# Performance work log

Measured on AMD Instinct MI355X. Metric: run time of the kernel, lower is better.

Reference implementation:

```python
import jax, jax.numpy as jnp
import numpy as np

L, H, D, HS = 6, 8, 512, 64
EPS = 1e-5


def _ln(x, g, b):
    m = jnp.mean(x, -1, keepdims=True)
    v = jnp.mean((x - m) ** 2, -1, keepdims=True)
    return (x - m) * jax.lax.rsqrt(v + EPS) * g + b


def _posenc(T, C):
    pos = jnp.arange(T, dtype=jnp.float32)[:, None]
    div = jnp.exp(jnp.arange(0, C, 2, dtype=jnp.float32) * (-jnp.log(10000.0) / C))
    pe = jnp.zeros((T, C), jnp.float32)
    pe = pe.at[:, 0::2].set(jnp.sin(pos * div))
    pe = pe.at[:, 1::2].set(jnp.cos(pos * div))
    return pe


def setup_inputs() -> dict:
    B, T, F, V, E, O = 8, 1024, 32, 7, 16, 49
    key = jax.random.key(0)
    ks = jax.random.split(key, 16)
    s = 0.02
    inp = {
        'code': jax.random.randint(ks[0], (B, T, F), 0, V),
        'lengths': jax.random.randint(ks[1], (B,), T // 2, T + 1),
        'emb': s * jax.random.normal(ks[2], (V, E), jnp.float32),
        'Wq': s * jax.random.normal(ks[3], (L, H, D, HS), jnp.float32),
        'Wk': s * jax.random.normal(ks[4], (L, H, D, HS), jnp.float32),
        'Wv': s * jax.random.normal(ks[5], (L, H, D, HS), jnp.float32),
        'Wo': s * jax.random.normal(ks[6], (L, D, D), jnp.float32),
        'bo': jnp.zeros((L, D), jnp.float32),
        'W1': s * jax.random.normal(ks[7], (L, D, 4 * D), jnp.float32),
        'b1': jnp.zeros((L, 4 * D), jnp.float32),
        'W2': s * jax.random.normal(ks[8], (L, 4 * D, D), jnp.float32),
        'b2': jnp.zeros((L, D), jnp.float32),
        'ln1_g': jnp.ones((L, D), jnp.float32),
        'ln1_b': jnp.zeros((L, D), jnp.float32),
        'ln2_g': jnp.ones((L, D), jnp.float32),
        'ln2_b': jnp.zeros((L, D), jnp.float32),
        'lnf_g': jnp.ones((D,), jnp.float32),
        'lnf_b': jnp.zeros((D,), jnp.float32),
        'attn_w': s * jax.random.normal(ks[9], (D, 1), jnp.float32),
        'attn_b': jnp.zeros((1,), jnp.float32),
        'head_w': s * jax.random.normal(ks[10], (D, 49), jnp.float32),
        'head_b': jnp.zeros((49,), jnp.float32),
    }
    return inp


def reference(code, lengths, emb, Wq, Wk, Wv, Wo, bo, W1, b1, W2, b2,
              ln1_g, ln1_b, ln2_g, ln2_b, lnf_g, lnf_b,
              attn_w, attn_b, head_w, head_b):
    B, T, F = code.shape
    # token embedding (B,T,F,E) -> (B,T,D) plus sinusoidal positions
    x = emb[code].reshape(B, T, D) + _posenc(T, D)
    mask = jnp.arange(T) < lengths[:, None]          # (B,T) valid positions
    col_mask = mask[:, None, None, :]                # mask key columns
    row_mask = mask[:, None, :, None]                # zero padded query rows
    for l in range(L):
        xn = _ln(x, ln1_g[l], ln1_b[l])
        q = jnp.einsum('btd,hde->bhte', xn, Wq[l])
        k = jnp.einsum('btd,hde->bhte', xn, Wk[l])
        v = jnp.einsum('btd,hde->bhte', xn, Wv[l])
        wei = jnp.einsum('bhte,bhse->bhts', q, k) * (HS ** -0.5)
        wei = jnp.where(col_mask, wei, -jnp.inf)
        wei = jax.nn.softmax(wei, axis=-1)
        wei = jnp.where(row_mask, wei, 0.0)
        o = jnp.einsum('bhts,bhse->bthe', wei, v).reshape(B, T, H * HS)
        x = x + o @ Wo[l] + bo[l]
        xn = _ln(x, ln2_g[l], ln2_b[l])
        x = x + jax.nn.gelu(xn @ W1[l] + b1[l], approximate=False) @ W2[l] + b2[l]
    x = _ln(x, lnf_g, lnf_b)
    # attention pooling over time
    scores = x @ attn_w + attn_b                     # (B,T,1)
    scores = jnp.where(mask[:, :, None], scores, -jnp.inf)
    aw = jax.nn.softmax(scores, axis=1)
    summary = jnp.sum(aw * x, axis=1)                # (B,D)
    logits = summary @ head_w + head_b               # (B,49)
    return logits
```

## Files before the change

kernel.cpp:

```cpp
#include <hip/hip_runtime.h>
#include <math.h>

#define TT 1024
#define BB 8
#define DD 512
#define HH 8
#define HSZ 64
#define LL 6
#define FF4 2048

typedef __attribute__((ext_vector_type(8))) short short8;
typedef __attribute__((ext_vector_type(4))) float floatx4;
typedef unsigned short ushort_t;
typedef unsigned int uint_t;

__device__ __forceinline__ ushort_t f2bf(float f) {
  uint_t u = __float_as_uint(f);
  u += 0x7fff + ((u >> 16) & 1);
  return (ushort_t)(u >> 16);
}
__device__ __forceinline__ float bf2f(ushort_t h) {
  return __uint_as_float(((uint_t)h) << 16);
}

typedef const __attribute__((address_space(1))) uint_t* gas_t;
typedef __attribute__((address_space(3))) uint_t* las_t;
__device__ __forceinline__ void stage16(const ushort_t* g, ushort_t* l) {
  __builtin_amdgcn_global_load_lds((gas_t)g, (las_t)l, 16, 0, 0);
}

#define VMWAIT(n) asm volatile("s_waitcnt vmcnt(" #n ")" ::: "memory")
#define MEMFENCE() asm volatile("" ::: "memory")


__global__ __launch_bounds__(256) void k_embed(const int* __restrict__ code,
                                               const float* __restrict__ emb,
                                               float* __restrict__ x,
                                               const int* __restrict__ lengths) {
  int idx = blockIdx.x * 256 + threadIdx.x;
  int c = idx & (DD - 1);
  int bt = idx >> 9;
  int t = bt & (TT - 1);
  if (t >= lengths[bt >> 10]) return;
  int f = c >> 4, e = c & 15;
  int vv = code[bt * 32 + f];
  int i = c >> 1;
  float freq = expf((float)(2 * i) * (-9.210340371976184f / 512.f));
  float ang = (float)t * freq;
  float pe = (c & 1) ? cosf(ang) : sinf(ang);
  x[idx] = emb[vv * 16 + e] + pe;
}

__global__ __launch_bounds__(256) void k_ln(const float* __restrict__ x,
                                            ushort_t* __restrict__ yB,
                                            float* __restrict__ yF,
                                            const float* __restrict__ g,
                                            const float* __restrict__ b,
                                            const float* __restrict__ aw,
                                            const float* __restrict__ ab,
                                            float* __restrict__ scores,
                                            const int* __restrict__ lengths) {
  int row0 = blockIdx.x * 4;
  if ((row0 & (TT - 1)) >= lengths[row0 >> 10]) return;
  int wave = threadIdx.x >> 6, lane = threadIdx.x & 63;
  int row = row0 + wave;
  const float* xr = x + (size_t)row * DD;
  float v[8];
  *(float4*)&v[0] = *(const float4*)(xr + lane * 8);
  *(float4*)&v[4] = *(const float4*)(xr + lane * 8 + 4);
  float s = 0.f;
#pragma unroll
  for (int j = 0; j < 8; ++j) s += v[j];
#pragma unroll
  for (int off = 32; off; off >>= 1) s += __shfl_down(s, off, 64);
  float mean = __shfl(s, 0, 64) * (1.f / DD);
  float qv = 0.f;
#pragma unroll
  for (int j = 0; j < 8; ++j) { float d = v[j] - mean; qv += d * d; }
#pragma unroll
  for (int off = 32; off; off >>= 1) qv += __shfl_down(qv, off, 64);
  float rs = rsqrtf(__shfl(qv, 0, 64) * (1.f / DD) + 1e-5f);
  float ov[8];
  float sdot = 0.f;
#pragma unroll
  for (int e = 0; e < 8; ++e) {
    int c = lane * 8 + e;
    ov[e] = (v[e] - mean) * rs * g[c] + b[c];
    if (scores) sdot += ov[e] * aw[c];
  }
  if (yB) {
    short8 o8;
#pragma unroll
    for (int e = 0; e < 8; ++e) o8[e] = (short)f2bf(ov[e]);
    size_t ad = (((size_t)(row >> 4) * 16 + (lane >> 2)) << 9) + ((lane & 3) * 16 + (row & 15)) * 8;
    *(short8*)(yB + ad) = o8;
  } else {
    float* yr = yF + (size_t)row * DD + lane * 8;
    *(float4*)yr = *(float4*)&ov[0];
    *(float4*)(yr + 4) = *(float4*)&ov[4];
  }
  if (scores) {
#pragma unroll
    for (int off = 32; off; off >>= 1) sdot += __shfl_down(sdot, off, 64);
    if (lane == 0) scores[row] = sdot + ab[0];
  }
}

__global__ __launch_bounds__(256) void k_packw(const float* __restrict__ in,
                                               ushort_t* __restrict__ out,
                                               int Nin, long in_ms, int nh,
                                               long os_l, int nblk, int Kout) {
  __shared__ float t4[64][65];
  int mz = blockIdx.z;
  const float* ip = in + (size_t)mz * in_ms;
  ushort_t* op = out + (size_t)(mz / nh) * os_l;
  int nbase = (mz % nh) * nblk + blockIdx.y * 64;
  int k0 = blockIdx.x * 64;
  int cc = threadIdx.x & 63, r0 = threadIdx.x >> 6;
#pragma unroll
  for (int i = 0; i < 16; ++i) {
    int r = r0 * 16 + i;
    t4[r][cc] = ip[(size_t)(k0 + r) * Nin + (nbase - (mz % nh) * nblk) + cc];
  }
  __syncthreads();
#pragma unroll
  for (int half = 0; half < 2; ++half) {
    int c = threadIdx.x + half * 256;
    int joct = c >> 6, nl = c & 63;
    int n = nbase + nl, k = k0 + joct * 8;
    short8 v8;
#pragma unroll
    for (int e = 0; e < 8; ++e) v8[e] = (short)f2bf(t4[joct * 8 + e][nl]);
    size_t ad = (((size_t)(n >> 4) * (Kout >> 5) + (k >> 5)) << 9) + (((k >> 3) & 3) * 16 + (n & 15)) * 8;
    *(short8*)(op + ad) = v8;
  }
}

template <int BM, int BN>
__global__ __launch_bounds__(256, (BM == 128) ? 3 : 4) void k_agemm(const ushort_t* __restrict__ Apk,
                                                                    const ushort_t* __restrict__ Bpk,
                                                                    const float* __restrict__ resid,
                                                                    const float* __restrict__ bias,
                                                                    float* __restrict__ outF,
                                                                    ushort_t* __restrict__ outB,
                                                                    int M, int N, int K, int mode,
                                                                    const int* __restrict__ lengths) {
  constexpr int MT = BM / 32;
  constexpr int NT = BN / 32;
  constexpr int NA = BM / 16;
  constexpr int NB = BN / 16;
  constexpr int NFRAG = NA + NB;
  constexpr int NF = NFRAG / 4;
  constexpr int BUFU = NFRAG * 512;
  constexpr int NBUF = (BM == 128) ? 2 : 4;
  __shared__ ushort_t lds[(BM == 128) ? 20480 : NBUF * BUFU];

  const int tid = threadIdx.x;
  const int w = tid >> 6, lane = tid & 63;
  const int quad = lane >> 4, l16 = lane & 15;
  const int gx = N / BN;
  int id = blockIdx.x;
  int bx = (id >> 3) % gx;
  int by = (id / (8 * gx)) * 8 + (id & 7);
  const int row0 = by * BM, col0 = bx * BN;
  if (lengths && (row0 & (TT - 1)) >= lengths[row0 >> 10]) return;
  const int nk = K >> 5;

  const int wrow0 = row0 + (w >> 1) * (BM / 2);
  const int wcol0 = col0 + (w & 1) * (BN / 2);
  const int ar16 = (w >> 1) * MT;
  const int bc16 = NA + (w & 1) * NT;

  const ushort_t* gsrc[NF];
  int slot[NF];
#pragma unroll
  for (int i = 0; i < NF; ++i) {
    int f = w * NF + i;
    if (f < NA)
      gsrc[i] = Apk + (((size_t)((row0 >> 4) + f) * nk) << 9) + lane * 8;
    else
      gsrc[i] = Bpk + (((size_t)((col0 >> 4) + (f - NA)) * nk) << 9) + lane * 8;
    slot[i] = f * 512;
  }

  floatx4 acc[MT][NT] = {};

  auto computeStep = [&](int bb) {
    const int base = bb * BUFU;
    short8 af[MT], bfv[NT];
#pragma unroll
    for (int mt = 0; mt < MT; ++mt) af[mt] = *(const short8*)&lds[base + (ar16 + mt) * 512 + lane * 8];
#pragma unroll
    for (int nt = 0; nt < NT; ++nt) bfv[nt] = *(const short8*)&lds[base + (bc16 + nt) * 512 + lane * 8];
#pragma unroll
    for (int mt = 0; mt < MT; ++mt)
#pragma unroll
      for (int nt = 0; nt < NT; ++nt)
        acc[mt][nt] = __builtin_amdgcn_mfma_f32_16x16x32_bf16(af[mt], bfv[nt], acc[mt][nt], 0, 0, 0);
  };

#pragma unroll
  for (int p = 0; p < NBUF - 1; ++p)
#pragma unroll
    for (int i = 0; i < NF; ++i)
      stage16(gsrc[i] + ((size_t)p << 9), &lds[p * BUFU + slot[i]]);

  int kc = 0;
  for (; kc + NBUF - 1 < nk; ++kc) {
    const int sslot = (kc + NBUF - 1) & (NBUF - 1);
#pragma unroll
    for (int i = 0; i < NF; ++i)
      stage16(gsrc[i] + ((size_t)(kc + NBUF - 1) << 9), &lds[sslot * BUFU + slot[i]]);
    if constexpr (BM == 128) VMWAIT(4);
    else VMWAIT(6);
    __builtin_amdgcn_s_barrier();
    MEMFENCE();
    computeStep(kc & (NBUF - 1));
    MEMFENCE();
    __builtin_amdgcn_s_barrier();
  }
  if constexpr (NBUF == 2) {
    VMWAIT(0);
    __builtin_amdgcn_s_barrier();
    MEMFENCE();
    computeStep(kc & 1);
  } else {
    VMWAIT(4);
    __builtin_amdgcn_s_barrier();
    MEMFENCE();
    computeStep(kc & 3);
    VMWAIT(2);
    __builtin_amdgcn_s_barrier();
    MEMFENCE();
    computeStep((kc + 1) & 3);
    VMWAIT(0);
    __builtin_amdgcn_s_barrier();
    MEMFENCE();
    computeStep((kc + 2) & 3);
  }

  if (BM == 128 && mode == 2) {
    __syncthreads();
    ushort_t* Cb = &lds[w * 5120];
#pragma unroll
    for (int mt = 0; mt < MT; ++mt)
#pragma unroll
      for (int nt = 0; nt < NT; ++nt) {
        floatx4 a4 = acc[mt][nt];
#pragma unroll
        for (int r = 0; r < 4; ++r) {
          float val = a4[r] + bias[wcol0 + nt * 16 + l16];
          val = 0.5f * val * (1.f + erff(val * 0.7071067811865475f));
          Cb[(mt * 16 + quad * 4 + r) * 80 + nt * 16 + l16] = f2bf(val);
        }
      }
#pragma unroll
    for (int mt2 = 0; mt2 < 4; ++mt2)
#pragma unroll
      for (int kt2 = 0; kt2 < 2; ++kt2) {
        short8 v8 = *(const short8*)&Cb[(mt2 * 16 + l16) * 80 + kt2 * 32 + quad * 8];
        size_t ad = ((((size_t)(wrow0 >> 4) + mt2) * (N >> 5) + (wcol0 >> 5) + kt2) << 9) + lane * 8;
        *(short8*)(outB + ad) = v8;
      }
  } else {
    const float qscale = (mode == 3 && col0 < 512) ? 0.125f : 1.0f;
#pragma unroll
    for (int mt = 0; mt < MT; ++mt)
#pragma unroll
      for (int nt = 0; nt < NT; ++nt) {
        floatx4 a4 = acc[mt][nt];
#pragma unroll
        for (int r = 0; r < 4; ++r) {
          int row = wrow0 + mt * 16 + quad * 4 + r;
          int col = wcol0 + nt * 16 + l16;
          float val = a4[r];
          if (bias) val += bias[col];
          size_t idx = (size_t)row * N + col;
          if (mode == 1) outF[idx] = val + resid[idx];
          else outB[idx] = f2bf(val * qscale);
        }
      }
  }
}

__global__ __launch_bounds__(256) void k_attn(const ushort_t* __restrict__ qkv,
                                              const int* __restrict__ lengths,
                                              ushort_t* __restrict__ o) {
  __shared__ ushort_t Ks[64 * 72];
  __shared__ ushort_t Vt[64 * 72];
  __shared__ ushort_t Ps[4][16 * 72];
  const int tid = threadIdx.x;
  const int w = tid >> 6, lane = tid & 63;
  const int quad = lane >> 4, l16 = lane & 15;
  const int tile = blockIdx.x & 15;
  const int bh = blockIdx.x >> 4;
  const int b = bh >> 3, h = bh & 7;
  const int len = lengths[b];
  if (tile * 64 >= len) return;
  const int tqa = tile * 64 + w * 16 + l16;
  const ushort_t* qp = qkv + ((size_t)(b * TT + tqa)) * 1536 + h * HSZ + quad * 8;
  short8 qf0 = *(const short8*)qp;
  short8 qf1 = *(const short8*)(qp + 32);
  floatx4 oacc[4] = {};
  float lsum[4] = {0.f, 0.f, 0.f, 0.f};
  const int skey = tid >> 2, sseg = (tid & 3) << 4;
  const int vkp = (tid & 31) << 1, vds = (tid >> 5) << 3;
  const int nkt = (len + 63) >> 6;
  for (int kt = 0; kt < nkt; ++kt) {
    const int s0 = kt * 64;
    __syncthreads();
    {
      const ushort_t* kp = qkv + ((size_t)(b * TT + s0 + skey)) * 1536 + 512 + h * HSZ + sseg;
      short8 k0 = *(const short8*)kp;
      short8 k1 = *(const short8*)(kp + 8);
      *(short8*)&Ks[skey * 72 + sseg] = k0;
      *(short8*)&Ks[skey * 72 + sseg + 8] = k1;
      const ushort_t* vp0 = qkv + ((size_t)(b * TT + s0 + vkp)) * 1536 + 1024 + h * HSZ + vds;
      short8 v0 = *(const short8*)vp0;
      short8 v1 = *(const short8*)(vp0 + 1536);
#pragma unroll
      for (int i = 0; i < 8; ++i) {
        ushort2 pr;
        pr.x = (ushort_t)v0[i];
        pr.y = (ushort_t)v1[i];
        *(ushort2*)&Vt[(vds + i) * 72 + vkp] = pr;
      }
    }
    __syncthreads();
    floatx4 sacc[4] = {};
#pragma unroll
    for (int nt = 0; nt < 4; ++nt) {
      short8 kf0 = *(const short8*)&Ks[(nt * 16 + l16) * 72 + quad * 8];
      short8 kf1 = *(const short8*)&Ks[(nt * 16 + l16) * 72 + 32 + quad * 8];
      sacc[nt] = __builtin_amdgcn_mfma_f32_16x16x32_bf16(qf0, kf0, sacc[nt], 0, 0, 0);
      sacc[nt] = __builtin_amdgcn_mfma_f32_16x16x32_bf16(qf1, kf1, sacc[nt], 0, 0, 0);
    }
    float p[4][4];
    if (kt == nkt - 1) {
#pragma unroll
      for (int nt = 0; nt < 4; ++nt) {
        bool valid = (s0 + nt * 16 + l16 < len);
#pragma unroll
        for (int r = 0; r < 4; ++r) p[nt][r] = valid ? __expf(sacc[nt][r]) : 0.f;
      }
    } else {
#pragma unroll
      for (int nt = 0; nt < 4; ++nt)
#pragma unroll
        for (int r = 0; r < 4; ++r) p[nt][r] = __expf(sacc[nt][r]);
    }
#pragma unroll
    for (int r = 0; r < 4; ++r)
#pragma unroll
      for (int nt = 0; nt < 4; ++nt) {
        lsum[r] += p[nt][r];
        Ps[w][(quad * 4 + r) * 72 + nt * 16 + l16] = f2bf(p[nt][r]);
      }
    short8 pf0 = *(const short8*)&Ps[w][l16 * 72 + quad * 8];
    short8 pf1 = *(const short8*)&Ps[w][l16 * 72 + 32 + quad * 8];
#pragma unroll
    for (int nt = 0; nt < 4; ++nt) {
      short8 vf0 = *(const short8*)&Vt[(nt * 16 + l16) * 72 + quad * 8];
      short8 vf1 = *(const short8*)&Vt[(nt * 16 + l16) * 72 + 32 + quad * 8];
      oacc[nt] = __builtin_amdgcn_mfma_f32_16x16x32_bf16(pf0, vf0, oacc[nt], 0, 0, 0);
      oacc[nt] = __builtin_amdgcn_mfma_f32_16x16x32_bf16(pf1, vf1, oacc[nt], 0, 0, 0);
    }
  }
#pragma unroll
  for (int off = 1; off < 16; off <<= 1) {
#pragma unroll
    for (int r = 0; r < 4; ++r) lsum[r] += __shfl_xor(lsum[r], off, 64);
  }
#pragma unroll
  for (int r = 0; r < 4; ++r) {
    int t = tile * 64 + w * 16 + quad * 4 + r;
    float inv = (t < len) ? 1.f / lsum[r] : 0.f;
#pragma unroll
    for (int nt = 0; nt < 4; ++nt)
      Ps[w][(quad * 4 + r) * 72 + nt * 16 + l16] = f2bf(oacc[nt][r] * inv);
  }
  const int mtile = b * 64 + tile * 4 + w;
#pragma unroll
  for (int kt2 = 0; kt2 < 2; ++kt2) {
    short8 v8 = *(const short8*)&Ps[w][l16 * 72 + kt2 * 32 + quad * 8];
    size_t ad = (((size_t)mtile * 16 + h * 2 + kt2) << 9) + lane * 8;
    *(short8*)(o + ad) = v8;
  }
}

__global__ __launch_bounds__(256) void k_softw(const float* __restrict__ scores,
                                               const int* __restrict__ lengths,
                                               float* __restrict__ wts) {
  __shared__ float red[8];
  int tid = threadIdx.x, b = blockIdx.x;
  int len = lengths[b];
  const float* sb = scores + b * TT;
  float m = -1e30f;
  for (int t = tid; t < len; t += 256) m = fmaxf(m, sb[t]);
#pragma unroll
  for (int off = 32; off; off >>= 1) m = fmaxf(m, __shfl_down(m, off, 64));
  if ((tid & 63) == 0) red[tid >> 6] = m;
  __syncthreads();
  m = fmaxf(fmaxf(red[0], red[1]), fmaxf(red[2], red[3]));
  float ssum = 0.f;
  for (int t = tid; t < len; t += 256) ssum += __expf(sb[t] - m);
#pragma unroll
  for (int off = 32; off; off >>= 1) ssum += __shfl_down(ssum, off, 64);
  if ((tid & 63) == 0) red[4 + (tid >> 6)] = ssum;
  __syncthreads();
  float inv = 1.f / (red[4] + red[5] + red[6] + red[7]);
  for (int t = tid; t < TT; t += 256)
    wts[b * TT + t] = (t < len) ? __expf(sb[t] - m) * inv : 0.f;
}

__global__ __launch_bounds__(256) void k_wsum(const float* __restrict__ xf,
                                              const float* __restrict__ wts,
                                              float* __restrict__ partial,
                                              const int* __restrict__ lengths) {
  int b = blockIdx.x, c = blockIdx.y, tid = threadIdx.x;
  float* pp = partial + ((size_t)b * 16 + c) * DD;
  if (c * 64 >= lengths[b]) {
    pp[tid] = 0.f;
    pp[tid + 256] = 0.f;
    return;
  }
  const float* xb = xf + ((size_t)b * TT + c * 64) * DD;
  const float* wb = wts + b * TT + c * 64;
  float a0 = 0.f, a1 = 0.f;
  for (int t = 0; t < 64; ++t) {
    float wv = wb[t];
    a0 += wv * xb[(size_t)t * DD + tid];
    a1 += wv * xb[(size_t)t * DD + tid + 256];
  }
  pp[tid] = a0;
  pp[tid + 256] = a1;
}

__global__ __launch_bounds__(64) void k_head(const float* __restrict__ partial,
                                             const float* __restrict__ head_w,
                                             const float* __restrict__ head_b,
                                             float* __restrict__ out) {
  __shared__ float ssum[DD];
  int b = blockIdx.x, tid = threadIdx.x;
  for (int d = tid; d < DD; d += 64) {
    float s = 0.f;
#pragma unroll
    for (int c = 0; c < 16; ++c) s += partial[((size_t)b * 16 + c) * DD + d];
    ssum[d] = s;
  }
  __syncthreads();
  if (tid < 49) {
    float s = head_b[tid];
    for (int d = 0; d < DD; ++d) s += ssum[d] * head_w[d * 49 + tid];
    out[b * 49 + tid] = s;
  }
}

extern "C" void kernel_launch(void* const* d_in, const int* in_sizes, int n_in,
                              void* d_out, int out_size, void* d_ws, size_t ws_size,
                              hipStream_t stream) {
  const int* code = (const int*)d_in[0];
  const int* lengths = (const int*)d_in[1];
  const float* emb = (const float*)d_in[2];
  const float* Wq = (const float*)d_in[3];
  const float* Wk = (const float*)d_in[4];
  const float* Wv = (const float*)d_in[5];
  const float* Wo = (const float*)d_in[6];
  const float* bo = (const float*)d_in[7];
  const float* W1 = (const float*)d_in[8];
  const float* b1 = (const float*)d_in[9];
  const float* W2 = (const float*)d_in[10];
  const float* b2 = (const float*)d_in[11];
  const float* ln1_g = (const float*)d_in[12];
  const float* ln1_b = (const float*)d_in[13];
  const float* ln2_g = (const float*)d_in[14];
  const float* ln2_b = (const float*)d_in[15];
  const float* lnf_g = (const float*)d_in[16];
  const float* lnf_b = (const float*)d_in[17];
  const float* attn_w = (const float*)d_in[18];
  const float* attn_b = (const float*)d_in[19];
  const float* head_w = (const float*)d_in[20];
  const float* head_b = (const float*)d_in[21];
  float* out = (float*)d_out;

  const size_t NTOK = (size_t)BB * TT;
  float* x = (float*)d_ws;
  ushort_t* xn = (ushort_t*)(x + NTOK * DD);
  ushort_t* un = xn + NTOK * DD;
  ushort_t* qkv = un;
  ushort_t* h1 = un;
  float* xf = (float*)un;
  ushort_t* wqpk = un + (size_t)NTOK * FF4;
  ushort_t* wopk = wqpk + (size_t)LL * 1536 * 512;
  ushort_t* w1pk = wopk + (size_t)LL * 512 * 512;
  ushort_t* w2pk = w1pk + (size_t)LL * 512 * FF4;
  float* scores = (float*)(w2pk + (size_t)LL * FF4 * 512);
  float* wts = scores + NTOK;
  float* partial = wts + NTOK;

  k_packw<<<dim3(8, 1, 48), 256, 0, stream>>>(Wq, wqpk,              64, (long)512 * 64, 8, (long)1536 * 512, 64, 512);
  k_packw<<<dim3(8, 1, 48), 256, 0, stream>>>(Wk, wqpk + 512 * 512,  64, (long)512 * 64, 8, (long)1536 * 512, 64, 512);
  k_packw<<<dim3(8, 1, 48), 256, 0, stream>>>(Wv, wqpk + 1024 * 512, 64, (long)512 * 64, 8, (long)1536 * 512, 64, 512);
  k_packw<<<dim3(8, 8, 6), 256, 0, stream>>>(Wo, wopk, 512, (long)512 * 512, 1, (long)512 * 512, 0, 512);
  k_packw<<<dim3(8, 32, 6), 256, 0, stream>>>(W1, w1pk, 2048, (long)512 * 2048, 1, (long)2048 * 512, 0, 512);
  k_packw<<<dim3(32, 8, 6), 256, 0, stream>>>(W2, w2pk, 512, (long)2048 * 512, 1, (long)512 * 2048, 0, 2048);

  k_embed<<<dim3((unsigned)((NTOK * DD) / 256)), dim3(256), 0, stream>>>(code, emb, x, lengths);

  for (int l = 0; l < LL; ++l) {
    k_ln<<<dim3(NTOK / 4), 256, 0, stream>>>(x, xn, nullptr, ln1_g + l * DD, ln1_b + l * DD,
                                             nullptr, nullptr, nullptr, lengths);
    k_agemm<128, 128><<<dim3(768), 256, 0, stream>>>(xn, wqpk + (size_t)l * 1536 * 512, nullptr, nullptr,
                                                     nullptr, qkv, (int)NTOK, 1536, 512, 3, lengths);
    k_attn<<<dim3(BB * HH * (TT / 64)), 256, 0, stream>>>(qkv, lengths, xn);
    k_agemm<64, 64><<<dim3(1024), 256, 0, stream>>>(xn, wopk + (size_t)l * 512 * 512, x, bo + l * DD,
                                                    x, nullptr, (int)NTOK, 512, 512, 1, lengths);
    k_ln<<<dim3(NTOK / 4), 256, 0, stream>>>(x, xn, nullptr, ln2_g + l * DD, ln2_b + l * DD,
                                             nullptr, nullptr, nullptr, lengths);
    k_agemm<128, 128><<<dim3(1024), 256, 0, stream>>>(xn, w1pk + (size_t)l * 512 * FF4, nullptr, b1 + l * FF4,
                                                      nullptr, h1, (int)NTOK, FF4, 512, 2, lengths);
    k_agemm<64, 64><<<dim3(1024), 256, 0, stream>>>(h1, w2pk + (size_t)l * FF4 * 512, x, b2 + l * DD,
                                                    x, nullptr, (int)NTOK, 512, 2048, 1, lengths);
  }
  k_ln<<<dim3(NTOK / 4), 256, 0, stream>>>(x, nullptr, xf, lnf_g, lnf_b,
                                           attn_w, attn_b, scores, lengths);
  k_softw<<<dim3(BB), 256, 0, stream>>>(scores, lengths, wts);
  k_wsum<<<dim3(BB, 16), 256, 0, stream>>>(xf, wts, partial, lengths);
  k_head<<<dim3(BB), 64, 0, stream>>>(partial, head_w, head_b, out);
}
```

Baseline: 1.211 ms.

## Use 128x64 tiles for Wo/W2 GEMMs with uniform triple-buffered pipeline

```diff
diff --git a/kernel.cpp b/kernel.cpp
--- a/kernel.cpp
+++ b/kernel.cpp
@@ -137,7 +137,7 @@
 }
 
 template <int BM, int BN>
-__global__ __launch_bounds__(256, (BM == 128) ? 3 : 4) void k_agemm(const ushort_t* __restrict__ Apk,
+__global__ __launch_bounds__(256, (BN == 128) ? 3 : 4) void k_agemm(const ushort_t* __restrict__ Apk,
                                                                     const ushort_t* __restrict__ Bpk,
                                                                     const float* __restrict__ resid,
                                                                     const float* __restrict__ bias,
@@ -152,8 +152,8 @@
   constexpr int NFRAG = NA + NB;
   constexpr int NF = NFRAG / 4;
   constexpr int BUFU = NFRAG * 512;
-  constexpr int NBUF = (BM == 128) ? 2 : 4;
-  __shared__ ushort_t lds[(BM == 128) ? 20480 : NBUF * BUFU];
+  constexpr int NBUF = 3;
+  __shared__ ushort_t lds[NBUF * BUFU];
 
   const int tid = threadIdx.x;
   const int w = tid >> 6, lane = tid & 63;
@@ -205,41 +205,34 @@
     for (int i = 0; i < NF; ++i)
       stage16(gsrc[i] + ((size_t)p << 9), &lds[p * BUFU + slot[i]]);
 
+  int cs = 0, ss = NBUF - 1;
   int kc = 0;
   for (; kc + NBUF - 1 < nk; ++kc) {
-    const int sslot = (kc + NBUF - 1) & (NBUF - 1);
 #pragma unroll
     for (int i = 0; i < NF; ++i)
-      stage16(gsrc[i] + ((size_t)(kc + NBUF - 1) << 9), &lds[sslot * BUFU + slot[i]]);
-    if constexpr (BM == 128) VMWAIT(4);
+      stage16(gsrc[i] + ((size_t)(kc + NBUF - 1) << 9), &lds[ss * BUFU + slot[i]]);
+    if constexpr (NF == 4) VMWAIT(8);
     else VMWAIT(6);
     __builtin_amdgcn_s_barrier();
     MEMFENCE();
-    computeStep(kc & (NBUF - 1));
+    computeStep(cs);
     MEMFENCE();
     __builtin_amdgcn_s_barrier();
-  }
-  if constexpr (NBUF == 2) {
-    VMWAIT(0);
-    __builtin_amdgcn_s_barrier();
-    MEMFENCE();
-    computeStep(kc & 1);
-  } else {
-    VMWAIT(4);
-    __builtin_amdgcn_s_barrier();
-    MEMFENCE();
-    computeStep(kc & 3);
-    VMWAIT(2);
-    __builtin_amdgcn_s_barrier();
-    MEMFENCE();
-    computeStep((kc + 1) & 3);
-    VMWAIT(0);
-    __builtin_amdgcn_s_barrier();
-    MEMFENCE();
-    computeStep((kc + 2) & 3);
-  }
-
-  if (BM == 128 && mode == 2) {
+    cs = (cs + 1 == NBUF) ? 0 : cs + 1;
+    ss = (ss + 1 == NBUF) ? 0 : ss + 1;
+  }
+  if constexpr (NF == 4) VMWAIT(4);
+  else VMWAIT(3);
+  __builtin_amdgcn_s_barrier();
+  MEMFENCE();
+  computeStep(cs);
+  const int cs2 = (cs + 1 == NBUF) ? 0 : cs + 1;
+  VMWAIT(0);
+  __builtin_amdgcn_s_barrier();
+  MEMFENCE();
+  computeStep(cs2);
+
+  if (BN == 128 && mode == 2) {
     __syncthreads();
     ushort_t* Cb = &lds[w * 5120];
 #pragma unroll
@@ -513,13 +506,13 @@
     k_agemm<128, 128><<<dim3(768), 256, 0, stream>>>(xn, wqpk + (size_t)l * 1536 * 512, nullptr, nullptr,
                                                      nullptr, qkv, (int)NTOK, 1536, 512, 3, lengths);
     k_attn<<<dim3(BB * HH * (TT / 64)), 256, 0, stream>>>(qkv, lengths, xn);
-    k_agemm<64, 64><<<dim3(1024), 256, 0, stream>>>(xn, wopk + (size_t)l * 512 * 512, x, bo + l * DD,
+    k_agemm<128, 64><<<dim3(512), 256, 0, stream>>>(xn, wopk + (size_t)l * 512 * 512, x, bo + l * DD,
                                                     x, nullptr, (int)NTOK, 512, 512, 1, lengths);
     k_ln<<<dim3(NTOK / 4), 256, 0, stream>>>(x, xn, nullptr, ln2_g + l * DD, ln2_b + l * DD,
                                              nullptr, nullptr, nullptr, lengths);
     k_agemm<128, 128><<<dim3(1024), 256, 0, stream>>>(xn, w1pk + (size_t)l * 512 * FF4, nullptr, b1 + l * FF4,
                                                       nullptr, h1, (int)NTOK, FF4, 512, 2, lengths);
-    k_agemm<64, 64><<<dim3(1024), 256, 0, stream>>>(h1, w2pk + (size_t)l * FF4 * 512, x, b2 + l * DD,
+    k_agemm<128, 64><<<dim3(512), 256, 0, stream>>>(h1, w2pk + (size_t)l * FF4 * 512, x, b2 + l * DD,
                                                     x, nullptr, (int)NTOK, 512, 2048, 1, lengths);
   }
   k_ln<<<dim3(NTOK / 4), 256, 0, stream>>>(x, nullptr, xf, lnf_g, lnf_b,
```

Measured after the change: 1.296 ms. +7.0%, slower.

## Double-buffer K/V tiles in attention kernel and remap block order

Applied to the files above, without the earlier changes.

```diff
diff --git a/kernel.cpp b/kernel.cpp
--- a/kernel.cpp
+++ b/kernel.cpp
@@ -286,14 +286,15 @@
 __global__ __launch_bounds__(256) void k_attn(const ushort_t* __restrict__ qkv,
                                               const int* __restrict__ lengths,
                                               ushort_t* __restrict__ o) {
-  __shared__ ushort_t Ks[64 * 72];
-  __shared__ ushort_t Vt[64 * 72];
+  __shared__ ushort_t Ks[2][64 * 72];
+  __shared__ ushort_t Vt[2][64 * 72];
   __shared__ ushort_t Ps[4][16 * 72];
   const int tid = threadIdx.x;
   const int w = tid >> 6, lane = tid & 63;
   const int quad = lane >> 4, l16 = lane & 15;
-  const int tile = blockIdx.x & 15;
-  const int bh = blockIdx.x >> 4;
+  const int id = (blockIdx.x & 7) * 128 + (blockIdx.x >> 3);
+  const int tile = id & 15;
+  const int bh = id >> 4;
   const int b = bh >> 3, h = bh & 7;
   const int len = lengths[b];
   if (tile * 64 >= len) return;
@@ -306,32 +307,41 @@
   const int skey = tid >> 2, sseg = (tid & 3) << 4;
   const int vkp = (tid & 31) << 1, vds = (tid >> 5) << 3;
   const int nkt = (len + 63) >> 6;
+
+  short8 k0r, k1r, v0r, v1r;
+  auto loadKV = [&](int kt) {
+    const int s0 = kt * 64;
+    const ushort_t* kp = qkv + ((size_t)(b * TT + s0 + skey)) * 1536 + 512 + h * HSZ + sseg;
+    k0r = *(const short8*)kp;
+    k1r = *(const short8*)(kp + 8);
+    const ushort_t* vp0 = qkv + ((size_t)(b * TT + s0 + vkp)) * 1536 + 1024 + h * HSZ + vds;
+    v0r = *(const short8*)vp0;
+    v1r = *(const short8*)(vp0 + 1536);
+  };
+  auto writeKV = [&](int buf) {
+    *(short8*)&Ks[buf][skey * 72 + sseg] = k0r;
+    *(short8*)&Ks[buf][skey * 72 + sseg + 8] = k1r;
+#pragma unroll
+    for (int i = 0; i < 8; ++i) {
+      ushort2 pr;
+      pr.x = (ushort_t)v0r[i];
+      pr.y = (ushort_t)v1r[i];
+      *(ushort2*)&Vt[buf][(vds + i) * 72 + vkp] = pr;
+    }
+  };
+
+  loadKV(0);
+  writeKV(0);
+  __syncthreads();
+  int cur = 0;
   for (int kt = 0; kt < nkt; ++kt) {
     const int s0 = kt * 64;
-    __syncthreads();
-    {
-      const ushort_t* kp = qkv + ((size_t)(b * TT + s0 + skey)) * 1536 + 512 + h * HSZ + sseg;
-      short8 k0 = *(const short8*)kp;
-      short8 k1 = *(const short8*)(kp + 8);
-      *(short8*)&Ks[skey * 72 + sseg] = k0;
-      *(short8*)&Ks[skey * 72 + sseg + 8] = k1;
-      const ushort_t* vp0 = qkv + ((size_t)(b * TT + s0 + vkp)) * 1536 + 1024 + h * HSZ + vds;
-      short8 v0 = *(const short8*)vp0;
-      short8 v1 = *(const short8*)(vp0 + 1536);
-#pragma unroll
-      for (int i = 0; i < 8; ++i) {
-        ushort2 pr;
-        pr.x = (ushort_t)v0[i];
-        pr.y = (ushort_t)v1[i];
-        *(ushort2*)&Vt[(vds + i) * 72 + vkp] = pr;
-      }
-    }
-    __syncthreads();
+    if (kt + 1 < nkt) loadKV(kt + 1);
     floatx4 sacc[4] = {};
 #pragma unroll
     for (int nt = 0; nt < 4; ++nt) {
-      short8 kf0 = *(const short8*)&Ks[(nt * 16 + l16) * 72 + quad * 8];
-      short8 kf1 = *(const short8*)&Ks[(nt * 16 + l16) * 72 + 32 + quad * 8];
+      short8 kf0 = *(const short8*)&Ks[cur][(nt * 16 + l16) * 72 + quad * 8];
+      short8 kf1 = *(const short8*)&Ks[cur][(nt * 16 + l16) * 72 + 32 + quad * 8];
       sacc[nt] = __builtin_amdgcn_mfma_f32_16x16x32_bf16(qf0, kf0, sacc[nt], 0, 0, 0);
       sacc[nt] = __builtin_amdgcn_mfma_f32_16x16x32_bf16(qf1, kf1, sacc[nt], 0, 0, 0);
     }
@@ -360,10 +370,15 @@
     short8 pf1 = *(const short8*)&Ps[w][l16 * 72 + 32 + quad * 8];
 #pragma unroll
     for (int nt = 0; nt < 4; ++nt) {
-      short8 vf0 = *(const short8*)&Vt[(nt * 16 + l16) * 72 + quad * 8];
-      short8 vf1 = *(const short8*)&Vt[(nt * 16 + l16) * 72 + 32 + quad * 8];
+      short8 vf0 = *(const short8*)&Vt[cur][(nt * 16 + l16) * 72 + quad * 8];
+      short8 vf1 = *(const short8*)&Vt[cur][(nt * 16 + l16) * 72 + 32 + quad * 8];
       oacc[nt] = __builtin_amdgcn_mfma_f32_16x16x32_bf16(pf0, vf0, oacc[nt], 0, 0, 0);
       oacc[nt] = __builtin_amdgcn_mfma_f32_16x16x32_bf16(pf1, vf1, oacc[nt], 0, 0, 0);
+    }
+    if (kt + 1 < nkt) {
+      writeKV(cur ^ 1);
+      __syncthreads();
+      cur ^= 1;
     }
   }
 #pragma unroll
```

Result: slower. 1.262 ms (+4.3%).
